# Kernel tuning notes

Measured on AMD Instinct MI355X. Metric: run time of the kernel, lower is better.

## Reference

```python
import jax, jax.numpy as jnp
import numpy as np


def _conv_relu(x, w, b):
    # Conv2d ksize=5, stride=1, padding=2 (same), dilation=1, then ReLU
    y = jax.lax.conv_general_dilated(x, w, window_strides=(1, 1), padding=[(2, 2), (2, 2)],
                                     dimension_numbers=("NCHW", "OIHW", "NCHW"))
    return jax.nn.relu(y + b[None, :, None, None])


def setup_inputs():
    B, S, C, M, BERT = 4, 128, 49, 288, 768
    ks = jax.random.split(jax.random.key(0), 12)
    return {
        "bert_output": jax.random.normal(ks[0], (B, S, BERT), jnp.float32),
        "memory_embs": jax.random.normal(ks[1], (B, S, C, M), jnp.float32),
        "mem_length": jax.random.randint(ks[2], (B, S, 1), 0, C + 1).astype(jnp.int32),
        "cn_concept_weights": jax.random.normal(ks[3], (B, S, C), jnp.float32),
        "ignore_no_memory_token": 1,
        "concept_size": C,
        "W_lin1": jax.random.normal(ks[4], (M, BERT), jnp.float32) * 0.02,
        "b_lin1": jnp.zeros((M,), jnp.float32),
        "sentinel": jax.random.normal(ks[5], (M,), jnp.float32) * 0.02,
        "weight1": jax.random.normal(ks[6], (M, C + 1), jnp.float32) * 0.05,
        "weight2": jax.random.normal(ks[7], (M, C + 1), jnp.float32) * 0.05,
        "conv1_w": jax.random.normal(ks[8], (S, S, 5, 5), jnp.float32) * 0.02,
        "conv1_b": jnp.zeros((S,), jnp.float32),
        "conv2_w": jax.random.normal(ks[9], (S, S, 5, 5), jnp.float32) * 0.02,
        "conv2_b": jnp.zeros((S,), jnp.float32),
        "ln_g": jnp.ones((144,), jnp.float32),
        "ln_b": jnp.zeros((144,), jnp.float32),
        "W_out": jax.random.normal(ks[10], (300, 144), jnp.float32) * 0.05,
        "b_out": jnp.zeros((300,), jnp.float32),
    }


def reference(bert_output, memory_embs, mem_length, cn_concept_weights,
              ignore_no_memory_token, concept_size,
              W_lin1, b_lin1, sentinel, weight1, weight2,
              conv1_w, conv1_b, conv2_w, conv2_b, ln_g, ln_b, W_out, b_out):
    B, S, _ = bert_output.shape
    C = concept_size
    M = sentinel.shape[0]
    eb = bert_output @ W_lin1.T + b_lin1                                   # [B,S,M]
    # add_sentinel: prepend sentinel row, extended_memory [B,S,C+1,M]
    ext_mem = jnp.concatenate([jnp.broadcast_to(sentinel, (B, S, 1, M)), memory_embs], axis=2)
    # expanded_bert[b,s,t,:] = eb[b,t,:]; avoid materializing it via einsum
    attn_w = jnp.einsum("btm,bsjm->bstj", eb, ext_mem)                     # [B,S,S,C+1]
    score = attn_w.mean(axis=2)                                            # [B,S,C+1]
    ordinal = jnp.arange(C + 1, dtype=jnp.float32)
    score = score + (mem_length.astype(jnp.float32) < ordinal).astype(jnp.float32) * (-1e6)
    cw = jnp.concatenate([jnp.zeros((B, S, 1), jnp.float32), cn_concept_weights], axis=2)
    score = 0.7 * jax.nn.softmax(score, axis=2) + 0.3 * jax.nn.softmax(cw, axis=2)
    # top-k threshold mask (keep >= 5th largest), then softmax over masked scores
    thr = jax.lax.top_k(score, 5)[0][..., 4:5]
    score = score * (score >= thr).astype(score.dtype)
    att = jax.nn.softmax(score, axis=2)                                    # [B,S,C+1]
    # torch: matmul of att repeated along last dim with ext_mem
    # == att[...,i] * sum_j ext_mem[...,j,:]
    summ = att[..., None] * ext_mem.sum(axis=2)[:, :, None, :]             # [B,S,C+1,M]
    # einsum 'b s a m, n c -> b s n m' is an outer product of the a-sum with the c-sum
    t1 = summ.sum(axis=2)                                                  # [B,S,M]
    t2 = jnp.einsum("bst,btm->bsm", attn_w.sum(axis=3), eb)                # sum_a (AW^T @ EB)
    cwt = (weight1.sum(axis=1)[None, None, :, None] * t1[:, :, None, :]
           + weight2.sum(axis=1)[None, None, :, None] * t2[:, :, None, :])  # [B,S,M,M]
    cwt = jax.nn.softmax(jnp.tanh(cwt), axis=2)
    summ = jnp.einsum("bsam,bsmn->bsan", summ, cwt)                        # [B,S,C+1,M]
    # self_coding: conv(S->S) -> maxpool2 -> conv -> LayerNorm(144) -> mean over dim2 -> Linear(144,300)
    x = _conv_relu(summ, conv1_w, conv1_b)
    x = jax.lax.reduce_window(x, -jnp.inf, jax.lax.max, (1, 1, 2, 2), (1, 1, 2, 2), "VALID")
    x = _conv_relu(x, conv2_w, conv2_b)                                    # [B,S,(C+1)//2,144]
    mu = x.mean(axis=-1, keepdims=True)
    var = ((x - mu) ** 2).mean(axis=-1, keepdims=True)
    x = (x - mu) / jnp.sqrt(var + 1e-5) * ln_g + ln_b
    x = x.mean(axis=2)                                                     # [B,S,144]
    out = x @ W_out.T + b_out                                              # [B,S,300]
    if ignore_no_memory_token:
        out = out * (mem_length > 0).astype(out.dtype)                     # [B,S,1] broadcast
    return out
```

## Files before the change

kernel.cpp:

```cpp
#include <hip/hip_runtime.h>

#define B_    4
#define S_    128
#define BERT_ 768
#define C_    49
#define C1_   50
#define M_    288
#define HP_   25
#define WP_   144
#define NOUT_ 300

typedef short bf16x8 __attribute__((ext_vector_type(8)));
typedef short short4v __attribute__((ext_vector_type(4)));
typedef float f32x4 __attribute__((ext_vector_type(4)));

static __device__ __forceinline__ short f2bf(float f) {
  unsigned u = __float_as_uint(f);
  unsigned r = (u + 0x7fffu + ((u >> 16) & 1u)) >> 16;
  return (short)r;
}
static __device__ __forceinline__ float bf2f(short v) {
  return __uint_as_float(((unsigned)(unsigned short)v) << 16);
}
static __device__ __forceinline__ unsigned cvt_pk_bf16(float lo, float hi) {
  unsigned r;
  asm("v_cvt_pk_bf16_f32 %0, %1, %2" : "=v"(r) : "v"(lo), "v"(hi));
  return r;
}

static __device__ __forceinline__ void cast_body(const float* src, short* dst,
                                                 long loOff, int R, int Ks, int Kd, int idx)
{
  if (idx >= R * Kd) return;
  int k = idx % Kd, r = idx / Kd;
  short h = 0, l = 0;
  if (k < Ks) {
    float v = src[(long)r * Ks + k];
    h = f2bf(v);
    l = f2bf(v - bf2f(h));
  }
  dst[idx] = h;
  dst[idx + loOff] = l;
}
static __device__ __forceinline__ void wperm_body(const float* w, short* wq, int r)
{
  if (r >= 128 * 128) return;
  int o = r >> 7, ch = r & 127;
  int chq = ch >> 3, e = ch & 7;
  const float* src = &w[(long)r * 25];
#pragma unroll
  for (int tap = 0; tap < 25; ++tap)
    wq[(((long)(tap * 16 + chq)) * 128 + o) * 8 + e] = f2bf(src[tap]);
}
__global__ __launch_bounds__(256) void prep_kernel(
    const float* __restrict__ bert, short* __restrict__ bertb,
    const float* __restrict__ W1, short* __restrict__ w1b,
    const float* __restrict__ Wo, short* __restrict__ wob,
    const float* __restrict__ c1w, short* __restrict__ w1p,
    const float* __restrict__ c2w, short* __restrict__ w2p,
    const float* __restrict__ w1m, const float* __restrict__ w2m,
    float* __restrict__ w1s, float* __restrict__ w2s)
{
  const int g = blockIdx.x, tid = threadIdx.x;
  if (g < 1536)       cast_body(bert, bertb, 393216L, 512, 768, 768, g * 256 + tid);
  else if (g < 2400)  cast_body(W1, w1b, 221184L, 288, 768, 768, (g - 1536) * 256 + tid);
  else if (g < 2700)  cast_body(Wo, wob, 76800L, 300, 144, 256, (g - 2400) * 256 + tid);
  else if (g < 2764)  wperm_body(c1w, w1p, (g - 2700) * 256 + tid);
  else if (g < 2828)  wperm_body(c2w, w2p, (g - 2764) * 256 + tid);
  else {
    int m = (g - 2828) * 256 + tid;
    if (m < M_) {
      float a = 0.f, b = 0.f;
      for (int c = 0; c < C1_; ++c) { a += w1m[m * C1_ + c]; b += w2m[m * C1_ + c]; }
      w1s[m] = a; w2s[m] = b;
    }
  }
}

template<int OMODE>
__global__ __launch_bounds__(256) void gemm_split(
    const short* __restrict__ A, const short* __restrict__ Bm,
    const float* __restrict__ bias,
    float* __restrict__ Outf, short* __restrict__ Outb,
    int Mr, int Nc, int KH,
    long aB, int aP, long aLo,
    long bB, int bP, long bLo,
    long oB, int oP,
    long obB, int obP, long obLo,
    const int* __restrict__ ml, const int* __restrict__ ign)
{
  const int z = blockIdx.z;
  const int i0 = blockIdx.y * 64, j0 = blockIdx.x * 64;
  __shared__ __attribute__((aligned(16))) short As[2][64 * 64];
  __shared__ __attribute__((aligned(16))) short Bs[2][64 * 64];
  const int tid = threadIdx.x;
  const int wave = tid >> 6, lane = tid & 63;
  const int lr = lane & 15, kq = lane >> 4;
  f32x4 acc[4] = {};
  const short* Ab = A + z * aB;
  const short* Bb = Bm + z * bB;
  const bf16x8 vz = {0, 0, 0, 0, 0, 0, 0, 0};
  for (int kh = 0; kh < KH; ++kh) {
    if (kh) __syncthreads();
    for (int u = tid; u < 512; u += 256) {
      int row = u >> 3, c = u & 7;
      int gi = i0 + row;
      const short* src = &Ab[(long)gi * aP + kh * 64 + c * 8];
      bf16x8 vh = (gi < Mr) ? *(const bf16x8*)src : vz;
      bf16x8 vl = (gi < Mr) ? *(const bf16x8*)(src + aLo) : vz;
      int dst = row * 64 + ((c ^ (row & 7)) * 8);
      *(bf16x8*)&As[0][dst] = vh;
      *(bf16x8*)&As[1][dst] = vl;
    }
    for (int u = tid; u < 512; u += 256) {
      int row = u >> 3, c = u & 7;
      int gj = j0 + row;
      const short* src = &Bb[(long)gj * bP + kh * 64 + c * 8];
      bf16x8 vh = (gj < Nc) ? *(const bf16x8*)src : vz;
      bf16x8 vl = (gj < Nc) ? *(const bf16x8*)(src + bLo) : vz;
      int dst = row * 64 + ((c ^ (row & 7)) * 8);
      *(bf16x8*)&Bs[0][dst] = vh;
      *(bf16x8*)&Bs[1][dst] = vl;
    }
    __syncthreads();
#pragma unroll
    for (int ks = 0; ks < 2; ++ks) {
      const int ch = ks * 4 + kq;
      const int ar = wave * 16 + lr;
      const int ao = ar * 64 + ((ch ^ (ar & 7)) * 8);
      bf16x8 ah = *(const bf16x8*)&As[0][ao];
      bf16x8 al = *(const bf16x8*)&As[1][ao];
#pragma unroll
      for (int ni = 0; ni < 4; ++ni) {
        const int br = ni * 16 + lr;
        const int bo2 = br * 64 + ((ch ^ (br & 7)) * 8);
        bf16x8 bh = *(const bf16x8*)&Bs[0][bo2];
        bf16x8 bl = *(const bf16x8*)&Bs[1][bo2];
        acc[ni] = __builtin_amdgcn_mfma_f32_16x16x32_bf16(ah, bh, acc[ni], 0, 0, 0);
        acc[ni] = __builtin_amdgcn_mfma_f32_16x16x32_bf16(ah, bl, acc[ni], 0, 0, 0);
        acc[ni] = __builtin_amdgcn_mfma_f32_16x16x32_bf16(al, bh, acc[ni], 0, 0, 0);
      }
    }
  }
#pragma unroll
  for (int ni = 0; ni < 4; ++ni) {
    int jg = j0 + ni * 16 + lr;
    if (jg >= Nc) continue;
#pragma unroll
    for (int r = 0; r < 4; ++r) {
      int ig = i0 + wave * 16 + kq * 4 + r;
      if (ig >= Mr) continue;
      float v = acc[ni][r];
      if (bias) v += bias[jg];
      if constexpr (OMODE == 0)
        Outf[z * oB + (long)ig * oP + jg] = v;
      if constexpr (OMODE == 1) {
        long o = ((long)((ig >> 7) * 288 + jg)) * 128 + (ig & 127);
        short h = f2bf(v);
        Outb[o] = h;
        Outb[o + obLo] = f2bf(v - bf2f(h));
      }
      if constexpr (OMODE == 2) {
        long o = z * obB + (long)ig * obP + jg;
        short h = f2bf(v);
        Outb[o] = h;
        Outb[o + obLo] = f2bf(v - bf2f(h));
      }
      if constexpr (OMODE == 3) {
        if (ign[0] != 0 && ml[ig] <= 0) v = 0.f;
        Outf[z * oB + (long)ig * oP + jg] = v;
      }
    }
  }
}

__global__ __launch_bounds__(256) void ebbar_kernel(
    const short* __restrict__ ebt, float* __restrict__ ebb)
{
  int row = blockIdx.x * 256 + threadIdx.x;
  if (row >= 4 * M_) return;
  const short* hi = &ebt[(long)row * 128];
  const short* lo = hi + 147456;
  float s = 0.f;
#pragma unroll
  for (int q = 0; q < 16; ++q) {
    bf16x8 vh = *(const bf16x8*)&hi[q * 8];
    bf16x8 vl = *(const bf16x8*)&lo[q * 8];
#pragma unroll
    for (int e = 0; e < 8; ++e) s += bf2f(vh[e]) + bf2f(vl[e]);
  }
  ebb[row] = s * (1.f / (float)S_);
}

__global__ __launch_bounds__(256) void score_kernel(
    const float* __restrict__ mem, const float* __restrict__ sentinel,
    const float* __restrict__ ebbar, const float* __restrict__ cw,
    const int* __restrict__ ml, float* __restrict__ E, short* __restrict__ Eb,
    float* __restrict__ attTp)
{
  const int s = blockIdx.x, b = blockIdx.y;
  const int tid = threadIdx.x, wave = tid >> 6, lane = tid & 63;
  __shared__ float sEb[M_];
  __shared__ float sE[4][M_];
  __shared__ float sScore[C1_];
  for (int m = tid; m < M_; m += 256) sEb[m] = ebbar[b * M_ + m];
  __syncthreads();

  const float* base = mem + ((long)(b * S_ + s)) * C_ * M_;
  float Ereg[5] = {0.f, 0.f, 0.f, 0.f, 0.f};
  for (int jj = wave; jj < C_; jj += 4) {
    const float* row = base + (long)jj * M_;
    float d = 0.f;
#pragma unroll
    for (int q = 0; q < 5; ++q) {
      int m = lane + q * 64;
      if (m < M_) { float v = row[m]; Ereg[q] += v; d = fmaf(v, sEb[m], d); }
    }
#pragma unroll
    for (int off = 32; off; off >>= 1) d += __shfl_down(d, off, 64);
    if (lane == 0) sScore[jj + 1] = d;
  }
#pragma unroll
  for (int q = 0; q < 5; ++q) { int m = lane + q * 64; if (m < M_) sE[wave][m] = Ereg[q]; }
  __syncthreads();

  if (wave == 0) {
    float d0 = 0.f;
    for (int m = lane; m < M_; m += 64) d0 = fmaf(sentinel[m], sEb[m], d0);
#pragma unroll
    for (int off = 32; off; off >>= 1) d0 += __shfl_down(d0, off, 64);
    if (lane == 0) sScore[0] = d0;
  }
  for (int m = tid; m < M_; m += 256) {
    float ev = sentinel[m] + sE[0][m] + sE[1][m] + sE[2][m] + sE[3][m];
    E[((long)(b * S_ + s)) * M_ + m] = ev;
    short h = f2bf(ev);
    Eb[((long)(b * S_ + s)) * 384 + m] = h;
    Eb[196608 + ((long)(b * S_ + s)) * 384 + m] = f2bf(ev - bf2f(h));
  }
  __syncthreads();

  if (wave == 0) {
    const int mlv = ml[b * S_ + s];
    float sc = (lane < C1_) ? sScore[lane] : 0.f;
    if (lane < C1_ && mlv < lane) sc -= 1e6f;
    float mx = (lane < C1_) ? sc : -3.0e38f;
#pragma unroll
    for (int off = 32; off; off >>= 1) mx = fmaxf(mx, __shfl_xor(mx, off, 64));
    float e1 = (lane < C1_) ? __expf(sc - mx) : 0.f;
    float s1 = e1;
#pragma unroll
    for (int off = 32; off; off >>= 1) s1 += __shfl_xor(s1, off, 64);
    float p1 = e1 / s1;
    float cv = 0.f;
    if (lane >= 1 && lane < C1_) cv = cw[((long)(b * S_ + s)) * C_ + lane - 1];
    float mx2 = (lane < C1_) ? cv : -3.0e38f;
#pragma unroll
    for (int off = 32; off; off >>= 1) mx2 = fmaxf(mx2, __shfl_xor(mx2, off, 64));
    float e2 = (lane < C1_) ? __expf(cv - mx2) : 0.f;
    float s2 = e2;
#pragma unroll
    for (int off = 32; off; off >>= 1) s2 += __shfl_xor(s2, off, 64);
    float p2 = e2 / s2;
    float scm = 0.7f * p1 + 0.3f * p2;
    bool active = (lane < C1_);
    float thr = 0.f;
    for (int r = 0; r < 5; ++r) {
      float v = active ? scm : -3.0e38f;
      int idx = lane;
#pragma unroll
      for (int off = 32; off; off >>= 1) {
        float ov = __shfl_xor(v, off, 64);
        int oi = __shfl_xor(idx, off, 64);
        if (ov > v || (ov == v && oi < idx)) { v = ov; idx = oi; }
      }
      thr = v;
      if (lane == idx) active = false;
    }
    float kept = (lane < C1_ && scm >= thr) ? scm : 0.f;
    float mx3 = (lane < C1_) ? kept : -3.0e38f;
#pragma unroll
    for (int off = 32; off; off >>= 1) mx3 = fmaxf(mx3, __shfl_xor(mx3, off, 64));
    float e3 = (lane < C1_) ? __expf(kept - mx3) : 0.f;
    float s3 = e3;
#pragma unroll
    for (int off = 32; off; off >>= 1) s3 += __shfl_xor(s3, off, 64);
    if (lane < C1_) attTp[((long)(b * 54) + lane + 2) * 128 + s] = e3 / s3;
  }
}

__global__ __launch_bounds__(576) void g_aw_kernel(
    const float* __restrict__ E, const float* __restrict__ t2,
    const float* __restrict__ w1s, const float* __restrict__ w2s,
    short* __restrict__ Gt,
    const short* __restrict__ w1q, const float* __restrict__ attp,
    short* __restrict__ AWq)
{
  __shared__ float sE[M_], s1[M_], s2[M_];
  __shared__ float sAtt[5][128];
  const int gb = blockIdx.x;
  const int tid = threadIdx.x;

  if (gb < 512) {
    const int s = gb & 127, b = gb >> 7;
    const long base = (long)(b * S_ + s) * M_;
    for (int m = tid; m < M_; m += 576) { sE[m] = E[base + m]; s1[m] = w1s[m]; s2[m] = w2s[m]; }
    __syncthreads();
    const int n = tid >> 1, half = tid & 1;
    const float a = sE[n];
    const float c = t2[base + n];
    float num = 0.f, den = 0.f;
    const int m0 = half * 144;
#pragma unroll 4
    for (int mm = 0; mm < 144; ++mm) {
      int m = m0 + mm;
      float z = fmaf(s1[m], a, s2[m] * c);
      float u = __expf(2.f * z);
      float th = fmaf(-2.f, __builtin_amdgcn_rcpf(u + 1.f), 1.f);
      float e = __expf(th);
      num = fmaf(sE[m], e, num);
      den += e;
    }
    num += __shfl_xor(num, 1, 64);
    den += __shfl_xor(den, 1, 64);
    if (half == 0)
      Gt[((long)(b * 292) + 2 + n) * 128 + s] = f2bf(num / den);
  } else {
    const int j = gb - 512;
    const int half = j & 1;
    const int h = (j >> 1) % 50;
    const int b = (j >> 1) / 50;
    if (tid < 256) {
      for (int u = tid; u < 640; u += 256)
        sAtt[u >> 7][u & 127] = attp[((long)(b * 54) + h + (u >> 7)) * 128 + (u & 127)];
    }
    __syncthreads();
    if (tid < 256) {
      const long obase = ((long)(b * 50 + h) * 80) * 1024;
      for (int u = tid; u < 5120; u += 256) {
        int c = half * 40 + (u >> 7);
        int o = u & 127;
        int dw = c / 16, chq = c & 15;
        float acc[8] = {};
#pragma unroll
        for (int dh = 0; dh < 5; ++dh) {
          bf16x8 wv = *(const bf16x8*)&w1q[(((long)((dh * 5 + dw) * 16 + chq)) * 128 + o) * 8];
          const float* ar = &sAtt[dh][chq * 8];
#pragma unroll
          for (int e = 0; e < 8; ++e) acc[e] = fmaf(bf2f(wv[e]), ar[e], acc[e]);
        }
        union { unsigned u4[4]; bf16x8 v; } pk;
        pk.u4[0] = cvt_pk_bf16(acc[0], acc[1]);
        pk.u4[1] = cvt_pk_bf16(acc[2], acc[3]);
        pk.u4[2] = cvt_pk_bf16(acc[4], acc[5]);
        pk.u4[3] = cvt_pk_bf16(acc[6], acc[7]);
        *(bf16x8*)&AWq[obase + (long)c * 1024 + o * 8] = pk.v;
      }
    }
  }
}

__global__ __launch_bounds__(256) void conv1_mfma(
    const short* __restrict__ AWq, const short* __restrict__ Gt,
    const float* __restrict__ bias, short* __restrict__ y1t)
{
  const int b = blockIdx.z, hrow = blockIdx.y;
  const int w0 = blockIdx.x * 144;
  __shared__ __attribute__((aligned(16))) short Bs[2][148 * 64];
  const int tid = threadIdx.x;
  const int wave = tid >> 6, lane = tid & 63;
  const int lr = lane & 15, kq = lane >> 4;
  f32x4 acc[2][9] = {};

  const short* src = Gt + ((long)(b * 292) + w0) * 128;
  for (int u = tid; u < 2368; u += 256) {
    int row = u >> 4, c = u & 15;
    bf16x8 v = *(const bf16x8*)&src[row * 128 + c * 8];
    *(bf16x8*)&Bs[c >> 3][row * 64 + (((c & 7) ^ (row & 7)) * 8)] = v;
  }
  __syncthreads();

  const long awb = (long)(b * 50 + hrow) * 80;
  for (int dw = 0; dw < 5; ++dw) {
#pragma unroll
    for (int ks = 0; ks < 4; ++ks) {
      const int ch = ks * 4 + kq;
      const long abase = (awb + dw * 16 + ch) * 128 + wave * 32 + lr;
      bf16x8 af0 = *(const bf16x8*)&AWq[abase * 8];
      bf16x8 af1 = *(const bf16x8*)&AWq[(abase + 16) * 8];
      const int arr = ch >> 3, cc = ch & 7;
#pragma unroll
      for (int ni = 0; ni < 9; ++ni) {
        const int row = lr + ni * 16 + dw;
        bf16x8 bfr = *(const bf16x8*)&Bs[arr][row * 64 + ((cc ^ (row & 7)) * 8)];
        acc[0][ni] = __builtin_amdgcn_mfma_f32_16x16x32_bf16(af0, bfr, acc[0][ni], 0, 0, 0);
        acc[1][ni] = __builtin_amdgcn_mfma_f32_16x16x32_bf16(af1, bfr, acc[1][ni], 0, 0, 0);
      }
    }
  }
#pragma unroll
  for (int mi = 0; mi < 2; ++mi) {
    const int og = wave * 32 + mi * 16 + kq * 4;
#pragma unroll
    for (int ni = 0; ni < 9; ++ni) {
      int wg = w0 + ni * 16 + lr;
      short4v pk;
#pragma unroll
      for (int r = 0; r < 4; ++r)
        pk[r] = f2bf(fmaxf(acc[mi][ni][r] + bias[og + r], 0.f));
      *(short4v*)&y1t[(((long)(b * 50) + hrow) * 288 + wg) * 128 + og] = pk;
    }
  }
}

__global__ __launch_bounds__(256) void conv2_dh(
    const short* __restrict__ wq,
    const short* __restrict__ act,
    short* __restrict__ y2p)
{
  constexpr int NREP = 3;
  const int bz = blockIdx.z;
  const int b = bz / 5, dh = bz % 5;
  const int hp = blockIdx.y;
  const int w0 = blockIdx.x * 48;
  __shared__ __attribute__((aligned(16))) short Bs[2][52 * 64];
  const int tid = threadIdx.x;
  const int wave = tid >> 6, lane = tid & 63;
  const int lr = lane & 15, kq = lane >> 4;
  f32x4 acc[2][NREP] = {};

  const short* src = act + (((long)(b * 29) + hp + dh) * 148 + w0) * 128;
  for (int u = tid; u < 832; u += 256) {
    int row = u >> 4, c = u & 15;
    bf16x8 v = *(const bf16x8*)&src[row * 128 + c * 8];
    *(bf16x8*)&Bs[c >> 3][row * 64 + (((c & 7) ^ (row & 7)) * 8)] = v;
  }
  __syncthreads();

#pragma unroll
  for (int dw = 0; dw < 5; ++dw) {
    const int tap = dh * 5 + dw;
#pragma unroll
    for (int ks = 0; ks < 4; ++ks) {
      const int ch = ks * 4 + kq;
      const long abase = ((long)(tap * 16 + ch)) * 128 + wave * 32 + lr;
      bf16x8 af0 = *(const bf16x8*)&wq[abase * 8];
      bf16x8 af1 = *(const bf16x8*)&wq[(abase + 16) * 8];
      const int arr = ch >> 3, cc = ch & 7;
#pragma unroll
      for (int ni = 0; ni < NREP; ++ni) {
        const int row = lr + ni * 16 + dw;
        bf16x8 bfr = *(const bf16x8*)&Bs[arr][row * 64 + ((cc ^ (row & 7)) * 8)];
        acc[0][ni] = __builtin_amdgcn_mfma_f32_16x16x32_bf16(af0, bfr, acc[0][ni], 0, 0, 0);
        acc[1][ni] = __builtin_amdgcn_mfma_f32_16x16x32_bf16(af1, bfr, acc[1][ni], 0, 0, 0);
      }
    }
  }
#pragma unroll
  for (int mi = 0; mi < 2; ++mi) {
    const int og = wave * 32 + mi * 16 + kq * 4;
#pragma unroll
    for (int ni = 0; ni < NREP; ++ni) {
      int wg = w0 + ni * 16 + lr;
#pragma unroll
      for (int r = 0; r < 4; ++r)
        y2p[((long)(dh * 512 + b * 128 + og + r)) * 3600 + hp * 144 + wg] =
            f2bf(acc[mi][ni][r]);
    }
  }
}

__global__ __launch_bounds__(256) void tail_fuse(
    const short* __restrict__ y2p, const float* __restrict__ bias,
    const float* __restrict__ lng, const float* __restrict__ lnb,
    short* __restrict__ zb)
{
  const int o = blockIdx.x, b = blockIdx.y;
  const int tid = threadIdx.x, wave = tid >> 6, lane = tid & 63;
  __shared__ float sZ[4][3][64];
  float zacc[3] = {0.f, 0.f, 0.f};
  const float bo = bias[o];
  const long base = ((long)(b * 128 + o)) * 3600;
  for (int hp = wave; hp < HP_; hp += 4) {
    float v[3]; float s = 0.f, ss = 0.f;
#pragma unroll
    for (int q = 0; q < 3; ++q) {
      int wp = lane + q * 64;
      float x = 0.f;
      if (wp < WP_) {
        x = bo;
#pragma unroll
        for (int dh = 0; dh < 5; ++dh)
          x += bf2f(y2p[(long)dh * 512 * 3600 + base + hp * 144 + wp]);
        x = fmaxf(x, 0.f);
      }
      v[q] = x; s += x; ss = fmaf(x, x, ss);
    }
#pragma unroll
    for (int off = 32; off; off >>= 1) { s += __shfl_xor(s, off, 64); ss += __shfl_xor(ss, off, 64); }
    float mu = s * (1.f / (float)WP_);
    float var = ss * (1.f / (float)WP_) - mu * mu;
    float inv = rsqrtf(var + 1e-5f);
#pragma unroll
    for (int q = 0; q < 3; ++q) {
      int wp = lane + q * 64;
      if (wp < WP_) zacc[q] += (v[q] - mu) * inv * lng[wp] + lnb[wp];
    }
  }
#pragma unroll
  for (int q = 0; q < 3; ++q) sZ[wave][q][lane] = zacc[q];
  __syncthreads();
  if (wave == 0) {
#pragma unroll
    for (int q = 0; q < 3; ++q) {
      int wp = lane + q * 64;
      if (wp < WP_) {
        float z = (sZ[0][q][lane] + sZ[1][q][lane] + sZ[2][q][lane] + sZ[3][q][lane])
                  * (1.f / (float)HP_);
        long t = (long)(b * 128 + o);
        short h = f2bf(z);
        zb[t * 256 + wp] = h;
        zb[131072 + t * 256 + wp] = f2bf(z - bf2f(h));
      }
    }
  }
}

__global__ void pool_t(const short* __restrict__ y1t, short* __restrict__ x2t)
{
  int idx = blockIdx.x * 256 + threadIdx.x;
  if (idx >= B_ * HP_ * WP_ * 16) return;
  int c8 = idx & 15; int t = idx >> 4;
  int wp = t % WP_; t /= WP_;
  int hp = t % HP_; int b = t / HP_;
  const short* base = y1t + (((long)(b * 50 + 2 * hp) * 288) + 2 * wp) * 128 + c8 * 8;
  bf16x8 v00 = *(const bf16x8*)&base[0];
  bf16x8 v01 = *(const bf16x8*)&base[128];
  bf16x8 v10 = *(const bf16x8*)&base[288 * 128];
  bf16x8 v11 = *(const bf16x8*)&base[288 * 128 + 128];
  bf16x8 r;
#pragma unroll
  for (int e = 0; e < 8; ++e)
    r[e] = f2bf(fmaxf(fmaxf(bf2f(v00[e]), bf2f(v01[e])), fmaxf(bf2f(v10[e]), bf2f(v11[e]))));
  *(bf16x8*)&x2t[(((long)(b * 29) + hp + 2) * 148 + wp + 2) * 128 + c8 * 8] = r;
}

extern "C" void kernel_launch(void* const* d_in, const int* in_sizes, int n_in,
                              void* d_out, int out_size, void* d_ws, size_t ws_size,
                              hipStream_t stream)
{
  const float* bert = (const float*)d_in[0];
  const float* mem  = (const float*)d_in[1];
  const int*   ml   = (const int*)d_in[2];
  const float* cw   = (const float*)d_in[3];
  const int*   ign  = (const int*)d_in[4];
  const float* W1   = (const float*)d_in[6];
  const float* b1l  = (const float*)d_in[7];
  const float* sent = (const float*)d_in[8];
  const float* w1m  = (const float*)d_in[9];
  const float* w2m  = (const float*)d_in[10];
  const float* c1w  = (const float*)d_in[11];
  const float* c1b  = (const float*)d_in[12];
  const float* c2w  = (const float*)d_in[13];
  const float* c2b  = (const float*)d_in[14];
  const float* lng  = (const float*)d_in[15];
  const float* lnb  = (const float*)d_in[16];
  const float* Wo   = (const float*)d_in[17];
  const float* bo   = (const float*)d_in[18];
  float* out = (float*)d_out;

  short* Gt    = (short*)d_ws;
  short* x2t   = Gt + 149504;
  short* zb    = x2t + 2197504;
  float* attTp = (float*)(zb + 262144);
  float* w1s   = attTp + 27648;
  float* w2s   = w1s + 288;
  float* ebb   = w2s + 288;
  short* wob   = (short*)(ebb + 1152);
  short* w1p   = wob + 153600;
  short* w2p   = w1p + 409600;
  short* y1t   = w2p + 409600;
  short* poolX = y1t + 7372800;
  short* bertb = poolX;
  short* w1b   = bertb + 786432;
  short* ebt   = w1b + 442368;
  short* Eb    = ebt + 294912;
  short* pb    = Eb + 393216;
  float* E     = (float*)(pb + 884736);
  float* t2    = E + 147456;
  short* AWq   = poolX;
  short* y2p   = poolX;

  dim3 blk(256);

  hipMemsetAsync(Gt, 0, (size_t)5328896, stream);
  hipMemsetAsync(Eb, 0, (size_t)(393216 + 884736) * 2, stream);

  prep_kernel<<<dim3(2830), blk, 0, stream>>>(
      bert, bertb, W1, w1b, Wo, wob, c1w, w1p, c2w, w2p, w1m, w2m, w1s, w2s);

  gemm_split<1><<<dim3(5, 8, 1), blk, 0, stream>>>(
      bertb, w1b, b1l, (float*)nullptr, ebt, 512, 288, 12,
      0L, 768, 393216L, 0L, 768, 221184L, 0L, 288, 0L, 0, 147456L,
      (const int*)nullptr, (const int*)nullptr);

  ebbar_kernel<<<dim3(5), blk, 0, stream>>>(ebt, ebb);

  score_kernel<<<dim3(S_, B_), blk, 0, stream>>>(mem, sent, ebb, cw, ml, E, Eb, attTp);

  gemm_split<2><<<dim3(5, 5, 4), blk, 0, stream>>>(
      ebt, ebt, (const float*)nullptr, (float*)nullptr, pb, 288, 288, 2,
      (long)288 * 128, 128, 147456L, (long)288 * 128, 128, 147456L,
      0L, 0, (long)288 * 384, 384, 442368L,
      (const int*)nullptr, (const int*)nullptr);

  gemm_split<0><<<dim3(5, 2, 4), blk, 0, stream>>>(
      Eb, pb, (const float*)nullptr, t2, (short*)nullptr, 128, 288, 6,
      (long)128 * 384, 384, 196608L, (long)288 * 384, 384, 442368L,
      (long)128 * 288, 288, 0L, 0, 0L,
      (const int*)nullptr, (const int*)nullptr);

  g_aw_kernel<<<dim3(912), dim3(576), 0, stream>>>(
      E, t2, w1s, w2s, Gt, w1p, attTp, AWq);

  conv1_mfma<<<dim3(2, 50, 4), blk, 0, stream>>>(AWq, Gt, c1b, y1t);

  pool_t<<<dim3((B_ * HP_ * WP_ * 16 + 255) / 256), blk, 0, stream>>>(y1t, x2t);

  conv2_dh<<<dim3(3, 25, 20), blk, 0, stream>>>(w2p, x2t, y2p);

  tail_fuse<<<dim3(128, 4), blk, 0, stream>>>(y2p, c2b, lng, lnb, zb);

  gemm_split<3><<<dim3(5, 8, 1), blk, 0, stream>>>(
      zb, wob, bo, out, (short*)nullptr, 512, 300, 4,
      0L, 256, 131072L, 0L, 256, 76800L, 0L, 300, 0L, 0, 0L,
      ml, ign);
}
```

Baseline: 190.8 us.

## Merge score kernel and EB^T·EB split-bf16 GEMM into one launch

The score kernel and the per-batch EB^T·EB GEMM (previously a separate gemm_split<2> launch) now run in a single grid. Blocks 0-511 do the score/softmax work and blocks 512-611 each compute a 64x64 tile of the product with hi/lo bf16 MFMA, writing pb. This removes one kernel launch and lets the two independent jobs overlap on the GPU. The cost is higher LDS use per block from the GEMM staging buffers, which may lower occupancy for the memory-bound score blocks.

Result: faster. 184.3 us (-3.4%).

```diff
diff --git a/kernel.cpp b/kernel.cpp
--- a/kernel.cpp
+++ b/kernel.cpp
@@ -192,100 +192,178 @@
   ebb[row] = s * (1.f / (float)S_);
 }
 
-__global__ __launch_bounds__(256) void score_kernel(
+__global__ __launch_bounds__(256) void score_p_kernel(
     const float* __restrict__ mem, const float* __restrict__ sentinel,
     const float* __restrict__ ebbar, const float* __restrict__ cw,
     const int* __restrict__ ml, float* __restrict__ E, short* __restrict__ Eb,
-    float* __restrict__ attTp)
-{
-  const int s = blockIdx.x, b = blockIdx.y;
-  const int tid = threadIdx.x, wave = tid >> 6, lane = tid & 63;
+    float* __restrict__ attTp,
+    const short* __restrict__ ebt, short* __restrict__ pb)
+{
   __shared__ float sEb[M_];
   __shared__ float sE[4][M_];
   __shared__ float sScore[C1_];
-  for (int m = tid; m < M_; m += 256) sEb[m] = ebbar[b * M_ + m];
-  __syncthreads();
-
-  const float* base = mem + ((long)(b * S_ + s)) * C_ * M_;
-  float Ereg[5] = {0.f, 0.f, 0.f, 0.f, 0.f};
-  for (int jj = wave; jj < C_; jj += 4) {
-    const float* row = base + (long)jj * M_;
-    float d = 0.f;
-#pragma unroll
-    for (int q = 0; q < 5; ++q) {
-      int m = lane + q * 64;
-      if (m < M_) { float v = row[m]; Ereg[q] += v; d = fmaf(v, sEb[m], d); }
-    }
-#pragma unroll
-    for (int off = 32; off; off >>= 1) d += __shfl_down(d, off, 64);
-    if (lane == 0) sScore[jj + 1] = d;
-  }
-#pragma unroll
-  for (int q = 0; q < 5; ++q) { int m = lane + q * 64; if (m < M_) sE[wave][m] = Ereg[q]; }
-  __syncthreads();
-
-  if (wave == 0) {
-    float d0 = 0.f;
-    for (int m = lane; m < M_; m += 64) d0 = fmaf(sentinel[m], sEb[m], d0);
-#pragma unroll
-    for (int off = 32; off; off >>= 1) d0 += __shfl_down(d0, off, 64);
-    if (lane == 0) sScore[0] = d0;
-  }
-  for (int m = tid; m < M_; m += 256) {
-    float ev = sentinel[m] + sE[0][m] + sE[1][m] + sE[2][m] + sE[3][m];
-    E[((long)(b * S_ + s)) * M_ + m] = ev;
-    short h = f2bf(ev);
-    Eb[((long)(b * S_ + s)) * 384 + m] = h;
-    Eb[196608 + ((long)(b * S_ + s)) * 384 + m] = f2bf(ev - bf2f(h));
-  }
-  __syncthreads();
-
-  if (wave == 0) {
-    const int mlv = ml[b * S_ + s];
-    float sc = (lane < C1_) ? sScore[lane] : 0.f;
-    if (lane < C1_ && mlv < lane) sc -= 1e6f;
-    float mx = (lane < C1_) ? sc : -3.0e38f;
-#pragma unroll
-    for (int off = 32; off; off >>= 1) mx = fmaxf(mx, __shfl_xor(mx, off, 64));
-    float e1 = (lane < C1_) ? __expf(sc - mx) : 0.f;
-    float s1 = e1;
-#pragma unroll
-    for (int off = 32; off; off >>= 1) s1 += __shfl_xor(s1, off, 64);
-    float p1 = e1 / s1;
-    float cv = 0.f;
-    if (lane >= 1 && lane < C1_) cv = cw[((long)(b * S_ + s)) * C_ + lane - 1];
-    float mx2 = (lane < C1_) ? cv : -3.0e38f;
-#pragma unroll
-    for (int off = 32; off; off >>= 1) mx2 = fmaxf(mx2, __shfl_xor(mx2, off, 64));
-    float e2 = (lane < C1_) ? __expf(cv - mx2) : 0.f;
-    float s2 = e2;
-#pragma unroll
-    for (int off = 32; off; off >>= 1) s2 += __shfl_xor(s2, off, 64);
-    float p2 = e2 / s2;
-    float scm = 0.7f * p1 + 0.3f * p2;
-    bool active = (lane < C1_);
-    float thr = 0.f;
-    for (int r = 0; r < 5; ++r) {
-      float v = active ? scm : -3.0e38f;
-      int idx = lane;
-#pragma unroll
-      for (int off = 32; off; off >>= 1) {
-        float ov = __shfl_xor(v, off, 64);
-        int oi = __shfl_xor(idx, off, 64);
-        if (ov > v || (ov == v && oi < idx)) { v = ov; idx = oi; }
-      }
-      thr = v;
-      if (lane == idx) active = false;
-    }
-    float kept = (lane < C1_ && scm >= thr) ? scm : 0.f;
-    float mx3 = (lane < C1_) ? kept : -3.0e38f;
-#pragma unroll
-    for (int off = 32; off; off >>= 1) mx3 = fmaxf(mx3, __shfl_xor(mx3, off, 64));
-    float e3 = (lane < C1_) ? __expf(kept - mx3) : 0.f;
-    float s3 = e3;
-#pragma unroll
-    for (int off = 32; off; off >>= 1) s3 += __shfl_xor(s3, off, 64);
-    if (lane < C1_) attTp[((long)(b * 54) + lane + 2) * 128 + s] = e3 / s3;
+  __shared__ __attribute__((aligned(16))) short As[2][64 * 64];
+  __shared__ __attribute__((aligned(16))) short Bs[2][64 * 64];
+  const int gb = blockIdx.x;
+  const int tid = threadIdx.x, wave = tid >> 6, lane = tid & 63;
+
+  if (gb < 512) {
+    const int s = gb & 127, b = gb >> 7;
+    for (int m = tid; m < M_; m += 256) sEb[m] = ebbar[b * M_ + m];
+    __syncthreads();
+
+    const float* base = mem + ((long)(b * S_ + s)) * C_ * M_;
+    float Ereg[5] = {0.f, 0.f, 0.f, 0.f, 0.f};
+    for (int jj = wave; jj < C_; jj += 4) {
+      const float* row = base + (long)jj * M_;
+      float d = 0.f;
+#pragma unroll
+      for (int q = 0; q < 5; ++q) {
+        int m = lane + q * 64;
+        if (m < M_) { float v = row[m]; Ereg[q] += v; d = fmaf(v, sEb[m], d); }
+      }
+#pragma unroll
+      for (int off = 32; off; off >>= 1) d += __shfl_down(d, off, 64);
+      if (lane == 0) sScore[jj + 1] = d;
+    }
+#pragma unroll
+    for (int q = 0; q < 5; ++q) { int m = lane + q * 64; if (m < M_) sE[wave][m] = Ereg[q]; }
+    __syncthreads();
+
+    if (wave == 0) {
+      float d0 = 0.f;
+      for (int m = lane; m < M_; m += 64) d0 = fmaf(sentinel[m], sEb[m], d0);
+#pragma unroll
+      for (int off = 32; off; off >>= 1) d0 += __shfl_down(d0, off, 64);
+      if (lane == 0) sScore[0] = d0;
+    }
+    for (int m = tid; m < M_; m += 256) {
+      float ev = sentinel[m] + sE[0][m] + sE[1][m] + sE[2][m] + sE[3][m];
+      E[((long)(b * S_ + s)) * M_ + m] = ev;
+      short h = f2bf(ev);
+      Eb[((long)(b * S_ + s)) * 384 + m] = h;
+      Eb[196608 + ((long)(b * S_ + s)) * 384 + m] = f2bf(ev - bf2f(h));
+    }
+    __syncthreads();
+
+    if (wave == 0) {
+      const int mlv = ml[b * S_ + s];
+      float sc = (lane < C1_) ? sScore[lane] : 0.f;
+      if (lane < C1_ && mlv < lane) sc -= 1e6f;
+      float mx = (lane < C1_) ? sc : -3.0e38f;
+#pragma unroll
+      for (int off = 32; off; off >>= 1) mx = fmaxf(mx, __shfl_xor(mx, off, 64));
+      float e1 = (lane < C1_) ? __expf(sc - mx) : 0.f;
+      float s1 = e1;
+#pragma unroll
+      for (int off = 32; off; off >>= 1) s1 += __shfl_xor(s1, off, 64);
+      float p1 = e1 / s1;
+      float cv = 0.f;
+      if (lane >= 1 && lane < C1_) cv = cw[((long)(b * S_ + s)) * C_ + lane - 1];
+      float mx2 = (lane < C1_) ? cv : -3.0e38f;
+#pragma unroll
+      for (int off = 32; off; off >>= 1) mx2 = fmaxf(mx2, __shfl_xor(mx2, off, 64));
+      float e2 = (lane < C1_) ? __expf(cv - mx2) : 0.f;
+      float s2 = e2;
+#pragma unroll
+      for (int off = 32; off; off >>= 1) s2 += __shfl_xor(s2, off, 64);
+      float p2 = e2 / s2;
+      float scm = 0.7f * p1 + 0.3f * p2;
+      bool active = (lane < C1_);
+      float thr = 0.f;
+      for (int r = 0; r < 5; ++r) {
+        float v = active ? scm : -3.0e38f;
+        int idx = lane;
+#pragma unroll
+        for (int off = 32; off; off >>= 1) {
+          float ov = __shfl_xor(v, off, 64);
+          int oi = __shfl_xor(idx, off, 64);
+          if (ov > v || (ov == v && oi < idx)) { v = ov; idx = oi; }
+        }
+        thr = v;
+        if (lane == idx) active = false;
+      }
+      float kept = (lane < C1_ && scm >= thr) ? scm : 0.f;
+      float mx3 = (lane < C1_) ? kept : -3.0e38f;
+#pragma unroll
+      for (int off = 32; off; off >>= 1) mx3 = fmaxf(mx3, __shfl_xor(mx3, off, 64));
+      float e3 = (lane < C1_) ? __expf(kept - mx3) : 0.f;
+      float s3 = e3;
+#pragma unroll
+      for (int off = 32; off; off >>= 1) s3 += __shfl_xor(s3, off, 64);
+      if (lane < C1_) attTp[((long)(b * 54) + lane + 2) * 128 + s] = e3 / s3;
+    }
+  } else {
+    const int j = gb - 512;
+    const int z = j / 25, rem = j % 25;
+    const int i0 = (rem / 5) * 64, j0 = (rem % 5) * 64;
+    const int lr = lane & 15, kq = lane >> 4;
+    const bf16x8 vz = {0, 0, 0, 0, 0, 0, 0, 0};
+    f32x4 acc[4] = {};
+    const short* Ab = ebt + (long)z * 36864;
+    for (int kh = 0; kh < 2; ++kh) {
+      if (kh) __syncthreads();
+      for (int u = tid; u < 512; u += 256) {
+        int row = u >> 3, c = u & 7;
+        int gi = i0 + row;
+        bf16x8 vh = vz, vl = vz;
+        if (gi < M_) {
+          const short* src = &Ab[(long)gi * 128 + kh * 64 + c * 8];
+          vh = *(const bf16x8*)src;
+          vl = *(const bf16x8*)(src + 147456);
+        }
+        int dst = row * 64 + ((c ^ (row & 7)) * 8);
+        *(bf16x8*)&As[0][dst] = vh;
+        *(bf16x8*)&As[1][dst] = vl;
+      }
+      for (int u = tid; u < 512; u += 256) {
+        int row = u >> 3, c = u & 7;
+        int gj = j0 + row;
+        bf16x8 vh = vz, vl = vz;
+        if (gj < M_) {
+          const short* src = &Ab[(long)gj * 128 + kh * 64 + c * 8];
+          vh = *(const bf16x8*)src;
+          vl = *(const bf16x8*)(src + 147456);
+        }
+        int dst = row * 64 + ((c ^ (row & 7)) * 8);
+        *(bf16x8*)&Bs[0][dst] = vh;
+        *(bf16x8*)&Bs[1][dst] = vl;
+      }
+      __syncthreads();
+#pragma unroll
+      for (int ks = 0; ks < 2; ++ks) {
+        const int ch = ks * 4 + kq;
+        const int ar = wave * 16 + lr;
+        const int ao = ar * 64 + ((ch ^ (ar & 7)) * 8);
+        bf16x8 ah = *(const bf16x8*)&As[0][ao];
+        bf16x8 al = *(const bf16x8*)&As[1][ao];
+#pragma unroll
+        for (int ni = 0; ni < 4; ++ni) {
+          const int br = ni * 16 + lr;
+          const int bo2 = br * 64 + ((ch ^ (br & 7)) * 8);
+          bf16x8 bh = *(const bf16x8*)&Bs[0][bo2];
+          bf16x8 bl = *(const bf16x8*)&Bs[1][bo2];
+          acc[ni] = __builtin_amdgcn_mfma_f32_16x16x32_bf16(ah, bh, acc[ni], 0, 0, 0);
+          acc[ni] = __builtin_amdgcn_mfma_f32_16x16x32_bf16(ah, bl, acc[ni], 0, 0, 0);
+          acc[ni] = __builtin_amdgcn_mfma_f32_16x16x32_bf16(al, bh, acc[ni], 0, 0, 0);
+        }
+      }
+    }
+#pragma unroll
+    for (int ni = 0; ni < 4; ++ni) {
+      int jg = j0 + ni * 16 + lr;
+      if (jg >= M_) continue;
+#pragma unroll
+      for (int r = 0; r < 4; ++r) {
+        int ig = i0 + wave * 16 + kq * 4 + r;
+        if (ig >= M_) continue;
+        long o = (long)z * 110592 + (long)ig * 384 + jg;
+        float v = acc[ni][r];
+        short h = f2bf(v);
+        pb[o] = h;
+        pb[o + 442368] = f2bf(v - bf2f(h));
+      }
+    }
   }
 }
 
@@ -606,13 +684,8 @@
 
   ebbar_kernel<<<dim3(5), blk, 0, stream>>>(ebt, ebb);
 
-  score_kernel<<<dim3(S_, B_), blk, 0, stream>>>(mem, sent, ebb, cw, ml, E, Eb, attTp);
-
-  gemm_split<2><<<dim3(5, 5, 4), blk, 0, stream>>>(
-      ebt, ebt, (const float*)nullptr, (float*)nullptr, pb, 288, 288, 2,
-      (long)288 * 128, 128, 147456L, (long)288 * 128, 128, 147456L,
-      0L, 0, (long)288 * 384, 384, 442368L,
-      (const int*)nullptr, (const int*)nullptr);
+  score_p_kernel<<<dim3(612), blk, 0, stream>>>(
+      mem, sent, ebb, cw, ml, E, Eb, attTp, ebt, pb);
 
   gemm_split<0><<<dim3(5, 2, 4), blk, 0, stream>>>(
       Eb, pb, (const float*)nullptr, t2, (short*)nullptr, 128, 288, 6,
```
